# Performance work log

Hardware: AMD Instinct MI355X
Metric: run time of the kernel (lower is better)

## Reference

```python
import jax, jax.numpy as jnp
import numpy as np

NEG_SLOPE = 0.2  # PyG GATConv default negative_slope


def gat_conv(x, src, dst, W, a_src, a_dst, b, n_nodes):
    # x: [N, Cin]; W: [H, Cin, Cout]; a_src/a_dst: [H, Cout]; b: [Cout]
    xh = jnp.einsum('ni,hio->nho', x, W)                 # [N, H, Cout]
    al_s = jnp.einsum('nho,ho->nh', xh, a_src)           # [N, H]
    al_d = jnp.einsum('nho,ho->nh', xh, a_dst)           # [N, H]
    e = jax.nn.leaky_relu(al_s[src] + al_d[dst], NEG_SLOPE)  # [E, H]
    # softmax over incoming edges of each dst node (self-loops guarantee >=1 edge)
    m = jax.ops.segment_max(e, dst, num_segments=n_nodes)
    ex = jnp.exp(e - m[dst])
    den = jax.ops.segment_sum(ex, dst, num_segments=n_nodes)
    alpha = ex / den[dst]                                # [E, H]
    msg = alpha[:, :, None] * xh[src]                    # [E, H, Cout]
    out = jax.ops.segment_sum(msg, dst, num_segments=n_nodes)  # [N, H, Cout]
    return out.mean(axis=1) + b                          # concat=False -> head mean


def setup_inputs() -> dict:
    key = jax.random.key(0)
    ks = jax.random.split(key, 16)
    N, E, C, H = 20000, 320000, 128, 4
    s = 1.0 / np.sqrt(C)
    inp = {
        'x': jax.random.normal(ks[0], (N, C), dtype=jnp.float32),
        'edge_index': jax.random.randint(ks[1], (2, E), 0, N, dtype=jnp.int64),
    }
    for i, name in enumerate(['1', '2', 'r']):
        k0, k1, k2 = jax.random.split(ks[2 + i], 3)
        inp['W' + name] = jax.random.normal(k0, (H, C, C), dtype=jnp.float32) * s
        inp['as' + name] = jax.random.normal(k1, (H, C), dtype=jnp.float32) * s
        inp['ad' + name] = jax.random.normal(k2, (H, C), dtype=jnp.float32) * s
        inp['b' + name] = jnp.zeros((C,), dtype=jnp.float32)
    return inp


def reference(x, edge_index, W1, as1, ad1, b1, W2, as2, ad2, b2, Wr, asr, adr, br):
    n = x.shape[0]
    loop = jnp.arange(n, dtype=edge_index.dtype)
    src = jnp.concatenate([edge_index[0], loop])  # PyG add_self_loops=True
    dst = jnp.concatenate([edge_index[1], loop])
    h = gat_conv(x, src, dst, W1, as1, ad1, b1, n)
    h = gat_conv(h, src, dst, W2, as2, ad2, b2, n)
    res = gat_conv(x, src, dst, Wr, asr, adr, br, n)
    return h + res
```

## Files before the change

kernel.cpp:

```cpp
#include <hip/hip_runtime.h>
#include <math.h>

#define C 128

typedef unsigned short u16;
typedef __attribute__((ext_vector_type(8))) short short8;
typedef __attribute__((ext_vector_type(4))) float f32x4;
typedef __attribute__((ext_vector_type(4))) u16 u16x4;

__device__ __forceinline__ float b2f(u16 u) {
    union { unsigned i; float f; } x; x.i = (unsigned)u << 16; return x.f;
}
__device__ __forceinline__ u16 f2b(float f) {
    union { float f; unsigned i; } x; x.f = f;
    unsigned r = x.i + 0x7FFFu + ((x.i >> 16) & 1u);
    return (u16)(r >> 16);
}
__device__ __forceinline__ float lrelu(float x) { return x > 0.f ? x : 0.2f * x; }


__global__ void hist_kernel(const int* __restrict__ ei, int E, int N,
                            int* __restrict__ count) {
    int total = E + N;
    for (int e = blockIdx.x * blockDim.x + threadIdx.x; e < total;
         e += gridDim.x * blockDim.x) {
        int d = (e < E) ? ei[E + e] : (e - E);
        if ((unsigned)d < (unsigned)N) atomicAdd(&count[d], 1);
    }
}

__global__ __launch_bounds__(1024) void scan_kernel(const int* __restrict__ count,
                                                    int* __restrict__ offs,
                                                    int* __restrict__ cursor, int N) {
    int tid = threadIdx.x, lane = tid & 63, wid = tid >> 6;
    int CH = (N + 1023) >> 10;
    int base = tid * CH;
    int s = 0;
    for (int j = 0; j < CH; ++j) {
        int i = base + j;
        if (i < N) s += count[i];
    }
    int own = s;
    #pragma unroll
    for (int d = 1; d < 64; d <<= 1) {
        int v = __shfl_up(s, d);
        if (lane >= d) s += v;
    }
    __shared__ int wtot[16];
    if (lane == 63) wtot[wid] = s;
    __syncthreads();
    if (tid < 16) {
        int t = wtot[tid];
        int u = t;
        #pragma unroll
        for (int d = 1; d < 16; d <<= 1) {
            int v = __shfl_up(u, d);
            if (tid >= d) u += v;
        }
        wtot[tid] = u - t;
        if (tid == 15) offs[N] = u;
    }
    __syncthreads();
    int run = wtot[wid] + s - own;
    for (int j = 0; j < CH; ++j) {
        int i = base + j;
        if (i < N) {
            offs[i] = run;
            cursor[i] = run;
            run += count[i];
        }
    }
}

__global__ void scatter_kernel(const int* __restrict__ ei, int E, int N,
                               int* __restrict__ cursor, int* __restrict__ srcs,
                               int* __restrict__ dsts) {
    int total = E + N;
    for (int e = blockIdx.x * blockDim.x + threadIdx.x; e < total;
         e += gridDim.x * blockDim.x) {
        int sNode, d;
        if (e < E) { sNode = ei[e]; d = ei[E + e]; }
        else       { sNode = e - E; d = sNode; }
        if ((unsigned)d < (unsigned)N && (unsigned)sNode < (unsigned)N) {
            int pos = atomicAdd(&cursor[d], 1);
            srcs[pos] = sNode;
            dsts[pos] = d;
        }
    }
}


__global__ __launch_bounds__(256) void cvt_w_kernel(const float* __restrict__ W1,
                                                    const float* __restrict__ Wr,
                                                    const float* __restrict__ W2,
                                                    u16* __restrict__ Wf) {
    int idx = blockIdx.x * 256 + threadIdx.x;
    int lane = idx & 63;
    int kk = (idx >> 6) & 15;
    int t = (idx >> 10) & 7;
    int l = idx >> 13;
    if (l >= 3) return;
    const float* W = (l == 0) ? W1 : (l == 1) ? Wr : W2;
    int o = t * 16 + (lane & 15);
    int bk = kk * 32 + (lane >> 4) * 8;
    int h = bk >> 7, i0 = bk & 127;
    short8 v;
    #pragma unroll
    for (int j = 0; j < 8; ++j) {
        v[j] = (short)f2b(0.25f * W[((size_t)h * C + i0 + j) * C + o]);
    }
    *(short8*)(Wf + (size_t)idx * 8) = v;
}


__global__ __launch_bounds__(256) void wvec_kernel(const float* __restrict__ W1,
                                                   const float* __restrict__ as1,
                                                   const float* __restrict__ ad1,
                                                   const float* __restrict__ Wr,
                                                   const float* __restrict__ asr,
                                                   const float* __restrict__ adr,
                                                   const float* __restrict__ W2,
                                                   const float* __restrict__ as2,
                                                   const float* __restrict__ ad2,
                                                   u16* __restrict__ vsdA,
                                                   u16* __restrict__ vsdB) {
    int slot = blockIdx.x;
    const float* W  = (slot < 4) ? W1 : (slot < 8) ? Wr : W2;
    const float* s_ = (slot < 4) ? as1 : (slot < 8) ? asr : as2;
    const float* d_ = (slot < 4) ? ad1 : (slot < 8) ? adr : ad2;
    int h = slot & 3;
    int wave = threadIdx.x >> 6, lane = threadIdx.x & 63;
    int rbase = blockIdx.y * 32 + wave * 8;
    float as0 = s_[h * C + lane], as1v = s_[h * C + 64 + lane];
    float ad0 = d_[h * C + lane], ad1v = d_[h * C + 64 + lane];
    #pragma unroll
    for (int j = 0; j < 8; ++j) {
        int i = rbase + j;
        const float* Wrow = W + ((size_t)h * C + i) * C;
        float w0 = Wrow[lane], w1 = Wrow[64 + lane];
        float ps = w0 * as0 + w1 * as1v;
        float pd = w0 * ad0 + w1 * ad1v;
        #pragma unroll
        for (int m = 32; m; m >>= 1) {
            ps += __shfl_xor(ps, m);
            pd += __shfl_xor(pd, m);
        }
        if (lane == 0) {
            if (slot < 8) {
                vsdA[slot * C + i] = f2b(ps);
                vsdA[(8 + slot) * C + i] = f2b(pd);
            } else {
                vsdB[(slot - 8) * C + i] = f2b(ps);
                vsdB[(4 + (slot - 8)) * C + i] = f2b(pd);
            }
        }
    }
}


__global__ __launch_bounds__(256) void alA_kernel(const float* __restrict__ x,
                                                  const u16* __restrict__ vsd,
                                                  u16* __restrict__ xb,
                                                  float* __restrict__ als,
                                                  float* __restrict__ ald, int N) {
    int wave = threadIdx.x >> 6, lane = threadIdx.x & 63;
    int rowBase = blockIdx.x * 64 + wave * 16;
    int r = rowBase + (lane & 15);
    int rl = r < N ? r : N - 1;
    int kg = (lane >> 4) * 8;

    short8 a[4];
    #pragma unroll
    for (int t = 0; t < 4; ++t) {
        const float* xp = x + (size_t)rl * C + t * 32 + kg;
        float4 f0 = *(const float4*)xp;
        float4 f1 = *(const float4*)(xp + 4);
        short8 s;
        s[0] = f2b(f0.x); s[1] = f2b(f0.y); s[2] = f2b(f0.z); s[3] = f2b(f0.w);
        s[4] = f2b(f1.x); s[5] = f2b(f1.y); s[6] = f2b(f1.z); s[7] = f2b(f1.w);
        a[t] = s;
        if (r < N) *(short8*)(xb + (size_t)r * C + t * 32 + kg) = s;
    }
    f32x4 acc = {0.f, 0.f, 0.f, 0.f};
    int col = lane & 15;
    #pragma unroll
    for (int t = 0; t < 4; ++t) {
        short8 b = *(const short8*)(vsd + (size_t)col * C + t * 32 + kg);
        acc = __builtin_amdgcn_mfma_f32_16x16x32_bf16(a[t], b, acc, 0, 0, 0);
    }
    #pragma unroll
    for (int j = 0; j < 4; ++j) {
        int rr = rowBase + (lane >> 4) * 4 + j;
        if (rr < N) {
            if (col < 8) als[rr * 8 + col] = acc[j];
            else ald[rr * 8 + (col - 8)] = acc[j];
        }
    }
}


__global__ __launch_bounds__(256) void alB_kernel(const u16* __restrict__ in,
                                                  const u16* __restrict__ vsd,
                                                  float* __restrict__ als,
                                                  float* __restrict__ ald, int N) {
    int wave = threadIdx.x >> 6, lane = threadIdx.x & 63;
    int rowBase = blockIdx.x * 64 + wave * 16;
    int r = rowBase + (lane & 15);
    int rl = r < N ? r : N - 1;
    int kg = (lane >> 4) * 8;

    f32x4 acc = {0.f, 0.f, 0.f, 0.f};
    int col = lane & 15;
    #pragma unroll
    for (int t = 0; t < 4; ++t) {
        short8 a = *(const short8*)(in + (size_t)rl * C + t * 32 + kg);
        short8 b = *(const short8*)(vsd + (size_t)col * C + t * 32 + kg);
        acc = __builtin_amdgcn_mfma_f32_16x16x32_bf16(a, b, acc, 0, 0, 0);
    }
    #pragma unroll
    for (int j = 0; j < 4; ++j) {
        int rr = rowBase + (lane >> 4) * 4 + j;
        if (rr < N && col < 8) {
            if (col < 4) als[rr * 4 + col] = acc[j];
            else ald[rr * 4 + (col - 4)] = acc[j];
        }
    }
}


template <int NH>
__global__ __launch_bounds__(256) void ew_kernel(const float* __restrict__ als,
                                                 const float* __restrict__ ald,
                                                 const int* __restrict__ srcs,
                                                 const int* __restrict__ dsts,
                                                 float* __restrict__ wout, int ET) {
    int i = blockIdx.x * blockDim.x + threadIdx.x;
    if (i >= ET) return;
    int s = srcs[i], d = dsts[i];
    const float* as_ = als + (size_t)s * NH;
    const float* ad_ = ald + (size_t)d * NH;
    float* wo = wout + (size_t)i * NH;
    #pragma unroll
    for (int h = 0; h < NH; ++h) {
        wo[h] = __expf(lrelu(as_[h] + ad_[h]));
    }
}


template <int NH>
__global__ __launch_bounds__(256) void aggx_kernel(const u16* __restrict__ xsrc,
                                                   const float* __restrict__ wgt,
                                                   const int* __restrict__ offs,
                                                   const int* __restrict__ srcs,
                                                   u16* __restrict__ dest, int N) {
    constexpr int NHG = NH / 2;
    int node = blockIdx.x * 4 + (threadIdx.x >> 6);
    int lane = threadIdx.x & 63;
    if (node >= N) return;
    int g = lane >> 5;
    int c0 = (lane & 31) * 4;
    int beg = offs[node], end = offs[node + 1];

    float dacc[NHG] = {};
    float acc[NHG][4] = {};

    int i = beg;
    int iend8 = beg + ((end - beg) & ~7);

    if (i < iend8) {
        int sA[8];
        #pragma unroll
        for (int e = 0; e < 8; ++e) sA[e] = srcs[i + e];
        while (i < iend8) {
            int inext = i + 8;
            int sB[8];
            #pragma unroll
            for (int e = 0; e < 8; ++e) sB[e] = srcs[inext + e];

            u16x4 v[8];
            #pragma unroll
            for (int e = 0; e < 8; ++e) {
                v[e] = *(const u16x4*)(xsrc + (size_t)sA[e] * C + c0);
            }
            float wv[8][NHG];
            #pragma unroll
            for (int e = 0; e < 8; ++e) {
                if constexpr (NHG == 4) {
                    float4 wq = *(const float4*)(wgt + (size_t)(i + e) * NH + g * NHG);
                    wv[e][0] = wq.x; wv[e][1] = wq.y; wv[e][2] = wq.z; wv[e][3] = wq.w;
                } else {
                    float2 wq = *(const float2*)(wgt + (size_t)(i + e) * NH + g * NHG);
                    wv[e][0] = wq.x; wv[e][1] = wq.y;
                }
            }
            #pragma unroll
            for (int e = 0; e < 8; ++e) {
                float f[4];
                #pragma unroll
                for (int j = 0; j < 4; ++j) f[j] = b2f(v[e][j]);
                #pragma unroll
                for (int j2 = 0; j2 < NHG; ++j2) {
                    dacc[j2] += wv[e][j2];
                    #pragma unroll
                    for (int j = 0; j < 4; ++j) acc[j2][j] += wv[e][j2] * f[j];
                }
            }
            #pragma unroll
            for (int e = 0; e < 8; ++e) sA[e] = sB[e];
            i = inext;
        }
    }
    for (; i < end; ++i) {
        int s0 = srcs[i];
        u16x4 v0 = *(const u16x4*)(xsrc + (size_t)s0 * C + c0);
        float w0[NHG];
        #pragma unroll
        for (int j2 = 0; j2 < NHG; ++j2) {
            w0[j2] = wgt[(size_t)i * NH + g * NHG + j2];
        }
        float f[4];
        #pragma unroll
        for (int j = 0; j < 4; ++j) f[j] = b2f(v0[j]);
        #pragma unroll
        for (int j2 = 0; j2 < NHG; ++j2) {
            dacc[j2] += w0[j2];
            #pragma unroll
            for (int j = 0; j < 4; ++j) acc[j2][j] += w0[j2] * f[j];
        }
    }

    #pragma unroll
    for (int j2 = 0; j2 < NHG; ++j2) {
        float inv = 1.f / dacc[j2];
        int h = g * NHG + j2;
        u16x4 o = {f2b(acc[j2][0] * inv), f2b(acc[j2][1] * inv),
                   f2b(acc[j2][2] * inv), f2b(acc[j2][3] * inv)};
        *(u16x4*)(dest + (size_t)node * (NH * C) + h * C + c0) = o;
    }
}


__global__ __launch_bounds__(256) void gemmL1_kernel(const u16* __restrict__ agg,
                                                     const u16* __restrict__ Wf,
                                                     const float* __restrict__ b1,
                                                     u16* __restrict__ h1b, int N) {
    int wave = threadIdx.x >> 6, lane = threadIdx.x & 63;
    int ch = blockIdx.y;
    int rowBase = blockIdx.x * 64 + wave * 16;
    int p = lane & 15, q = lane >> 4;
    int r = rowBase + p;
    int rl = r < N ? r : N - 1;
    int kg = q * 8;

    const short8* ap = (const short8*)(agg + (size_t)rl * 1024 + kg);
    const u16* wb = Wf + (size_t)(ch * 4 * 16) * 512 + lane * 8;

    f32x4 acc[4];
    #pragma unroll
    for (int t = 0; t < 4; ++t) acc[t] = (f32x4){0.f, 0.f, 0.f, 0.f};

    #pragma unroll
    for (int kk = 0; kk < 16; ++kk) {
        short8 a = ap[kk * 4];
        #pragma unroll
        for (int t = 0; t < 4; ++t) {
            short8 b = *(const short8*)(wb + (size_t)(t * 16 + kk) * 512);
            acc[t] = __builtin_amdgcn_mfma_f32_16x16x32_bf16(a, b, acc[t], 0, 0, 0);
        }
    }

    #pragma unroll
    for (int t = 0; t < 4; ++t) {
        int col = (ch * 4 + t) * 16 + p;
        float bcol = b1[col];
        #pragma unroll
        for (int j = 0; j < 4; ++j) {
            int rr = rowBase + q * 4 + j;
            if (rr < N) h1b[(size_t)rr * C + col] = f2b(acc[t][j] + bcol);
        }
    }
}


__global__ __launch_bounds__(256) void gemmF_kernel(const u16* __restrict__ aggB,
                                                    const u16* __restrict__ aggA,
                                                    const u16* __restrict__ Wf,
                                                    const float* __restrict__ b2,
                                                    const float* __restrict__ br,
                                                    float* __restrict__ outf, int N) {
    int wave = threadIdx.x >> 6, lane = threadIdx.x & 63;
    int ch = blockIdx.y;
    int rowBase = blockIdx.x * 64 + wave * 16;
    int p = lane & 15, q = lane >> 4;
    int r = rowBase + p;
    int rl = r < N ? r : N - 1;
    int kg = q * 8;

    const short8* apB = (const short8*)(aggB + (size_t)rl * 512 + kg);
    const short8* apR = (const short8*)(aggA + (size_t)rl * 1024 + 512 + kg);
    const u16* wb2 = Wf + (size_t)2 * 65536 + (size_t)(ch * 4 * 16) * 512 + lane * 8;
    const u16* wbr = Wf + (size_t)1 * 65536 + (size_t)(ch * 4 * 16) * 512 + lane * 8;

    f32x4 acc[4];
    #pragma unroll
    for (int t = 0; t < 4; ++t) acc[t] = (f32x4){0.f, 0.f, 0.f, 0.f};

    #pragma unroll
    for (int kk = 0; kk < 16; ++kk) {
        short8 a = apB[kk * 4];
        #pragma unroll
        for (int t = 0; t < 4; ++t) {
            short8 b = *(const short8*)(wb2 + (size_t)(t * 16 + kk) * 512);
            acc[t] = __builtin_amdgcn_mfma_f32_16x16x32_bf16(a, b, acc[t], 0, 0, 0);
        }
    }
    #pragma unroll
    for (int kk = 0; kk < 16; ++kk) {
        short8 a = apR[kk * 4];
        #pragma unroll
        for (int t = 0; t < 4; ++t) {
            short8 b = *(const short8*)(wbr + (size_t)(t * 16 + kk) * 512);
            acc[t] = __builtin_amdgcn_mfma_f32_16x16x32_bf16(a, b, acc[t], 0, 0, 0);
        }
    }

    #pragma unroll
    for (int t = 0; t < 4; ++t) {
        int col = (ch * 4 + t) * 16 + p;
        float bcol = b2[col] + br[col];
        #pragma unroll
        for (int j = 0; j < 4; ++j) {
            int rr = rowBase + q * 4 + j;
            if (rr < N) outf[(size_t)rr * C + col] = acc[t][j] + bcol;
        }
    }
}


extern "C" void kernel_launch(void* const* d_in, const int* in_sizes, int n_in,
                              void* d_out, int out_size, void* d_ws, size_t ws_size,
                              hipStream_t stream) {
    const float* x = (const float*)d_in[0];
    const int* ei = (const int*)d_in[1];
    const float* W1 = (const float*)d_in[2];
    const float* as1 = (const float*)d_in[3];
    const float* ad1 = (const float*)d_in[4];
    const float* b1 = (const float*)d_in[5];
    const float* W2 = (const float*)d_in[6];
    const float* as2 = (const float*)d_in[7];
    const float* ad2 = (const float*)d_in[8];
    const float* b2 = (const float*)d_in[9];
    const float* Wr = (const float*)d_in[10];
    const float* asr = (const float*)d_in[11];
    const float* adr = (const float*)d_in[12];
    const float* br = (const float*)d_in[13];

    int N = in_sizes[0] / C;
    int E = in_sizes[1] / 2;
    int ET = E + N;

    size_t sz_xb    = (size_t)N * C * 2;
    size_t sz_h1b   = (size_t)N * C * 2;
    size_t sz_aggA  = (size_t)N * 1024 * 2;
    size_t sz_aggB  = (size_t)N * 512 * 2;
    size_t sz_wc    = (size_t)3 * C * 512 * 2;
    size_t sz_vsd   = (size_t)16 * C * 2;
    size_t sz_al8   = (size_t)N * 8 * 4;
    size_t sz_count = (size_t)N * 4;
    size_t sz_offs  = (size_t)(N + 4) * 4;
    size_t sz_srcs  = (size_t)ET * 4;
    size_t sz_w     = (size_t)ET * 8 * 4;
    size_t required = sz_xb + sz_h1b + sz_aggA + sz_aggB + sz_wc + 2 * sz_vsd +
                      2 * sz_al8 + 2 * sz_count + sz_offs + 2 * sz_srcs + sz_w;
    if (ws_size < required) return;

    char* w = (char*)d_ws;
    u16* xb = (u16*)w;        w += sz_xb;
    u16* h1b = (u16*)w;       w += sz_h1b;
    u16* aggA = (u16*)w;      w += sz_aggA;
    u16* aggB = (u16*)w;      w += sz_aggB;
    u16* Wf = (u16*)w;        w += sz_wc;
    u16* vsdA = (u16*)w;      w += sz_vsd;
    u16* vsdB = (u16*)w;      w += sz_vsd;
    float* als = (float*)w;   w += sz_al8;
    float* ald = (float*)w;   w += sz_al8;
    int* count = (int*)w;     w += sz_count;
    int* cursor = (int*)w;    w += sz_count;
    int* offs = (int*)w;      w += sz_offs;
    int* srcs = (int*)w;      w += sz_srcs;
    int* dsts = (int*)w;      w += sz_srcs;
    float* wgt = (float*)w;   w += sz_w;
    float* out = (float*)d_out;

    hipMemsetAsync(count, 0, sz_count, stream);
    hist_kernel<<<512, 256, 0, stream>>>(ei, E, N, count);
    scan_kernel<<<1, 1024, 0, stream>>>(count, offs, cursor, N);
    scatter_kernel<<<512, 256, 0, stream>>>(ei, E, N, cursor, srcs, dsts);

    cvt_w_kernel<<<96, 256, 0, stream>>>(W1, Wr, W2, Wf);
    wvec_kernel<<<dim3(12, 4), 256, 0, stream>>>(W1, as1, ad1, Wr, asr, adr,
                                                 W2, as2, ad2, vsdA, vsdB);

    int nwb = (N + 3) / 4;
    int neb = (ET + 255) / 256;
    int gx = (N + 63) / 64;

    alA_kernel<<<gx, 256, 0, stream>>>(x, vsdA, xb, als, ald, N);
    ew_kernel<8><<<neb, 256, 0, stream>>>(als, ald, srcs, dsts, wgt, ET);
    aggx_kernel<8><<<nwb, 256, 0, stream>>>(xb, wgt, offs, srcs, aggA, N);
    gemmL1_kernel<<<dim3(gx, 2), 256, 0, stream>>>(aggA, Wf, b1, h1b, N);

    alB_kernel<<<gx, 256, 0, stream>>>(h1b, vsdB, als, ald, N);
    ew_kernel<4><<<neb, 256, 0, stream>>>(als, ald, srcs, dsts, wgt, ET);
    aggx_kernel<4><<<nwb, 256, 0, stream>>>(h1b, wgt, offs, srcs, aggB, N);
    gemmF_kernel<<<dim3(gx, 2), 256, 0, stream>>>(aggB, aggA, Wf, b2, br, out, N);
}
```

Baseline: 307.8 us.

## Fuse edge-weight computation into aggregation and merge prep kernels

Drops the separate per-edge weight kernels: the aggregation kernel now reads per-source attention logits and computes exp(leaky_relu(as+ad)) inline, so the dst array and the per-edge weight buffer are no longer needed. The weight conversion, attention-vector projection and count zeroing are merged into one prep kernel, replacing a memset and two launches. This avoids writing and re-reading an E×H float buffer and cuts launch count. In exchange the aggregation kernel does extra gathers of als rows and recomputes exp per lane group.

```diff
diff --git a/kernel.cpp b/kernel.cpp
--- a/kernel.cpp
+++ b/kernel.cpp
@@ -73,8 +73,7 @@
 }
 
 __global__ void scatter_kernel(const int* __restrict__ ei, int E, int N,
-                               int* __restrict__ cursor, int* __restrict__ srcs,
-                               int* __restrict__ dsts) {
+                               int* __restrict__ cursor, int* __restrict__ srcs) {
     int total = E + N;
     for (int e = blockIdx.x * blockDim.x + threadIdx.x; e < total;
          e += gridDim.x * blockDim.x) {
@@ -84,36 +83,12 @@
         if ((unsigned)d < (unsigned)N && (unsigned)sNode < (unsigned)N) {
             int pos = atomicAdd(&cursor[d], 1);
             srcs[pos] = sNode;
-            dsts[pos] = d;
-        }
-    }
-}
-
-
-__global__ __launch_bounds__(256) void cvt_w_kernel(const float* __restrict__ W1,
-                                                    const float* __restrict__ Wr,
-                                                    const float* __restrict__ W2,
-                                                    u16* __restrict__ Wf) {
-    int idx = blockIdx.x * 256 + threadIdx.x;
-    int lane = idx & 63;
-    int kk = (idx >> 6) & 15;
-    int t = (idx >> 10) & 7;
-    int l = idx >> 13;
-    if (l >= 3) return;
-    const float* W = (l == 0) ? W1 : (l == 1) ? Wr : W2;
-    int o = t * 16 + (lane & 15);
-    int bk = kk * 32 + (lane >> 4) * 8;
-    int h = bk >> 7, i0 = bk & 127;
-    short8 v;
-    #pragma unroll
-    for (int j = 0; j < 8; ++j) {
-        v[j] = (short)f2b(0.25f * W[((size_t)h * C + i0 + j) * C + o]);
-    }
-    *(short8*)(Wf + (size_t)idx * 8) = v;
-}
-
-
-__global__ __launch_bounds__(256) void wvec_kernel(const float* __restrict__ W1,
+        }
+    }
+}
+
+
+__global__ __launch_bounds__(256) void prep_kernel(const float* __restrict__ W1,
                                                    const float* __restrict__ as1,
                                                    const float* __restrict__ ad1,
                                                    const float* __restrict__ Wr,
@@ -122,38 +97,63 @@
                                                    const float* __restrict__ W2,
                                                    const float* __restrict__ as2,
                                                    const float* __restrict__ ad2,
+                                                   u16* __restrict__ Wf,
                                                    u16* __restrict__ vsdA,
-                                                   u16* __restrict__ vsdB) {
-    int slot = blockIdx.x;
-    const float* W  = (slot < 4) ? W1 : (slot < 8) ? Wr : W2;
-    const float* s_ = (slot < 4) ? as1 : (slot < 8) ? asr : as2;
-    const float* d_ = (slot < 4) ? ad1 : (slot < 8) ? adr : ad2;
-    int h = slot & 3;
-    int wave = threadIdx.x >> 6, lane = threadIdx.x & 63;
-    int rbase = blockIdx.y * 32 + wave * 8;
-    float as0 = s_[h * C + lane], as1v = s_[h * C + 64 + lane];
-    float ad0 = d_[h * C + lane], ad1v = d_[h * C + 64 + lane];
-    #pragma unroll
-    for (int j = 0; j < 8; ++j) {
-        int i = rbase + j;
-        const float* Wrow = W + ((size_t)h * C + i) * C;
-        float w0 = Wrow[lane], w1 = Wrow[64 + lane];
-        float ps = w0 * as0 + w1 * as1v;
-        float pd = w0 * ad0 + w1 * ad1v;
-        #pragma unroll
-        for (int m = 32; m; m >>= 1) {
-            ps += __shfl_xor(ps, m);
-            pd += __shfl_xor(pd, m);
-        }
-        if (lane == 0) {
-            if (slot < 8) {
-                vsdA[slot * C + i] = f2b(ps);
-                vsdA[(8 + slot) * C + i] = f2b(pd);
-            } else {
-                vsdB[(slot - 8) * C + i] = f2b(ps);
-                vsdB[(4 + (slot - 8)) * C + i] = f2b(pd);
+                                                   u16* __restrict__ vsdB,
+                                                   int* __restrict__ count, int N) {
+    int blk = blockIdx.x;
+    if (blk < 96) {
+        int idx = blk * 256 + threadIdx.x;
+        int lane = idx & 63;
+        int kk = (idx >> 6) & 15;
+        int t = (idx >> 10) & 7;
+        int l = idx >> 13;
+        const float* W = (l == 0) ? W1 : (l == 1) ? Wr : W2;
+        int o = t * 16 + (lane & 15);
+        int bk = kk * 32 + (lane >> 4) * 8;
+        int h = bk >> 7, i0 = bk & 127;
+        short8 v;
+        #pragma unroll
+        for (int j = 0; j < 8; ++j) {
+            v[j] = (short)f2b(0.25f * W[((size_t)h * C + i0 + j) * C + o]);
+        }
+        *(short8*)(Wf + (size_t)idx * 8) = v;
+    } else if (blk < 144) {
+        int b2 = blk - 96;
+        int slot = b2 >> 2;
+        const float* W  = (slot < 4) ? W1 : (slot < 8) ? Wr : W2;
+        const float* s_ = (slot < 4) ? as1 : (slot < 8) ? asr : as2;
+        const float* d_ = (slot < 4) ? ad1 : (slot < 8) ? adr : ad2;
+        int h = slot & 3;
+        int wave = threadIdx.x >> 6, lane = threadIdx.x & 63;
+        int rbase = (b2 & 3) * 32 + wave * 8;
+        float as0 = s_[h * C + lane], as1v = s_[h * C + 64 + lane];
+        float ad0 = d_[h * C + lane], ad1v = d_[h * C + 64 + lane];
+        #pragma unroll
+        for (int j = 0; j < 8; ++j) {
+            int i = rbase + j;
+            const float* Wrow = W + ((size_t)h * C + i) * C;
+            float w0 = Wrow[lane], w1 = Wrow[64 + lane];
+            float ps = w0 * as0 + w1 * as1v;
+            float pd = w0 * ad0 + w1 * ad1v;
+            #pragma unroll
+            for (int m = 32; m; m >>= 1) {
+                ps += __shfl_xor(ps, m);
+                pd += __shfl_xor(pd, m);
             }
-        }
+            if (lane == 0) {
+                if (slot < 8) {
+                    vsdA[slot * C + i] = f2b(ps);
+                    vsdA[(8 + slot) * C + i] = f2b(pd);
+                } else {
+                    vsdB[(slot - 8) * C + i] = f2b(ps);
+                    vsdB[(4 + (slot - 8)) * C + i] = f2b(pd);
+                }
+            }
+        }
+    } else {
+        int i = (blk - 144) * 256 + threadIdx.x;
+        if (i < N) count[i] = 0;
     }
 }
 
@@ -229,27 +229,9 @@
 
 
 template <int NH>
-__global__ __launch_bounds__(256) void ew_kernel(const float* __restrict__ als,
-                                                 const float* __restrict__ ald,
-                                                 const int* __restrict__ srcs,
-                                                 const int* __restrict__ dsts,
-                                                 float* __restrict__ wout, int ET) {
-    int i = blockIdx.x * blockDim.x + threadIdx.x;
-    if (i >= ET) return;
-    int s = srcs[i], d = dsts[i];
-    const float* as_ = als + (size_t)s * NH;
-    const float* ad_ = ald + (size_t)d * NH;
-    float* wo = wout + (size_t)i * NH;
-    #pragma unroll
-    for (int h = 0; h < NH; ++h) {
-        wo[h] = __expf(lrelu(as_[h] + ad_[h]));
-    }
-}
-
-
-template <int NH>
 __global__ __launch_bounds__(256) void aggx_kernel(const u16* __restrict__ xsrc,
-                                                   const float* __restrict__ wgt,
+                                                   const float* __restrict__ als,
+                                                   const float* __restrict__ ald,
                                                    const int* __restrict__ offs,
                                                    const int* __restrict__ srcs,
                                                    u16* __restrict__ dest, int N) {
@@ -261,6 +243,12 @@
     int c0 = (lane & 31) * 4;
     int beg = offs[node], end = offs[node + 1];
 
+    float adh[NHG];
+    #pragma unroll
+    for (int j = 0; j < NHG; ++j) {
+        adh[j] = ald[(size_t)node * NH + g * NHG + j];
+    }
+
     float dacc[NHG] = {};
     float acc[NHG][4] = {};
 
@@ -277,6 +265,17 @@
             #pragma unroll
             for (int e = 0; e < 8; ++e) sB[e] = srcs[inext + e];
 
+            float av[8][NHG];
+            #pragma unroll
+            for (int e = 0; e < 8; ++e) {
+                if constexpr (NHG == 4) {
+                    float4 t = *(const float4*)(als + (size_t)sA[e] * NH + g * NHG);
+                    av[e][0] = t.x; av[e][1] = t.y; av[e][2] = t.z; av[e][3] = t.w;
+                } else {
+                    float2 t = *(const float2*)(als + (size_t)sA[e] * NH + g * NHG);
+                    av[e][0] = t.x; av[e][1] = t.y;
+                }
+            }
             u16x4 v[8];
             #pragma unroll
             for (int e = 0; e < 8; ++e) {
@@ -285,12 +284,9 @@
             float wv[8][NHG];
             #pragma unroll
             for (int e = 0; e < 8; ++e) {
-                if constexpr (NHG == 4) {
-                    float4 wq = *(const float4*)(wgt + (size_t)(i + e) * NH + g * NHG);
-                    wv[e][0] = wq.x; wv[e][1] = wq.y; wv[e][2] = wq.z; wv[e][3] = wq.w;
-                } else {
-                    float2 wq = *(const float2*)(wgt + (size_t)(i + e) * NH + g * NHG);
-                    wv[e][0] = wq.x; wv[e][1] = wq.y;
+                #pragma unroll
+                for (int j2 = 0; j2 < NHG; ++j2) {
+                    wv[e][j2] = __expf(lrelu(av[e][j2] + adh[j2]));
                 }
             }
             #pragma unroll
@@ -313,19 +309,15 @@
     for (; i < end; ++i) {
         int s0 = srcs[i];
         u16x4 v0 = *(const u16x4*)(xsrc + (size_t)s0 * C + c0);
-        float w0[NHG];
+        float f[4];
+        #pragma unroll
+        for (int j = 0; j < 4; ++j) f[j] = b2f(v0[j]);
         #pragma unroll
         for (int j2 = 0; j2 < NHG; ++j2) {
-            w0[j2] = wgt[(size_t)i * NH + g * NHG + j2];
-        }
-        float f[4];
-        #pragma unroll
-        for (int j = 0; j < 4; ++j) f[j] = b2f(v0[j]);
-        #pragma unroll
-        for (int j2 = 0; j2 < NHG; ++j2) {
-            dacc[j2] += w0[j2];
-            #pragma unroll
-            for (int j = 0; j < 4; ++j) acc[j2][j] += w0[j2] * f[j];
+            float w0 = __expf(lrelu(als[(size_t)s0 * NH + g * NHG + j2] + adh[j2]));
+            dacc[j2] += w0;
+            #pragma unroll
+            for (int j = 0; j < 4; ++j) acc[j2][j] += w0 * f[j];
         }
     }
 
@@ -468,10 +460,9 @@
     size_t sz_al8   = (size_t)N * 8 * 4;
     size_t sz_count = (size_t)N * 4;
     size_t sz_offs  = (size_t)(N + 4) * 4;
-    size_t sz_srcs  = (size_t)ET * 4;
-    size_t sz_w     = (size_t)ET * 8 * 4;
+    size_t sz_srcs  = (size_t)ET * 4 + 64;
     size_t required = sz_xb + sz_h1b + sz_aggA + sz_aggB + sz_wc + 2 * sz_vsd +
-                      2 * sz_al8 + 2 * sz_count + sz_offs + 2 * sz_srcs + sz_w;
+                      2 * sz_al8 + 2 * sz_count + sz_offs + sz_srcs;
     if (ws_size < required) return;
 
     char* w = (char*)d_ws;
@@ -488,30 +479,24 @@
     int* cursor = (int*)w;    w += sz_count;
     int* offs = (int*)w;      w += sz_offs;
     int* srcs = (int*)w;      w += sz_srcs;
-    int* dsts = (int*)w;      w += sz_srcs;
-    float* wgt = (float*)w;   w += sz_w;
     float* out = (float*)d_out;
 
-    hipMemsetAsync(count, 0, sz_count, stream);
+    int nzb = (N + 255) / 256;
+    int nwb = (N + 3) / 4;
+    int gx = (N + 63) / 64;
+
+    prep_kernel<<<144 + nzb, 256, 0, stream>>>(W1, as1, ad1, Wr, asr, adr,
+                                               W2, as2, ad2, Wf, vsdA, vsdB,
+                                               count, N);
     hist_kernel<<<512, 256, 0, stream>>>(ei, E, N, count);
     scan_kernel<<<1, 1024, 0, stream>>>(count, offs, cursor, N);
-    scatter_kernel<<<512, 256, 0, stream>>>(ei, E, N, cursor, srcs, dsts);
-
-    cvt_w_kernel<<<96, 256, 0, stream>>>(W1, Wr, W2, Wf);
-    wvec_kernel<<<dim3(12, 4), 256, 0, stream>>>(W1, as1, ad1, Wr, asr, adr,
-                                                 W2, as2, ad2, vsdA, vsdB);
-
-    int nwb = (N + 3) / 4;
-    int neb = (ET + 255) / 256;
-    int gx = (N + 63) / 64;
+    scatter_kernel<<<512, 256, 0, stream>>>(ei, E, N, cursor, srcs);
 
     alA_kernel<<<gx, 256, 0, stream>>>(x, vsdA, xb, als, ald, N);
-    ew_kernel<8><<<neb, 256, 0, stream>>>(als, ald, srcs, dsts, wgt, ET);
-    aggx_kernel<8><<<nwb, 256, 0, stream>>>(xb, wgt, offs, srcs, aggA, N);
+    aggx_kernel<8><<<nwb, 256, 0, stream>>>(xb, als, ald, offs, srcs, aggA, N);
     gemmL1_kernel<<<dim3(gx, 2), 256, 0, stream>>>(aggA, Wf, b1, h1b, N);
 
     alB_kernel<<<gx, 256, 0, stream>>>(h1b, vsdB, als, ald, N);
-    ew_kernel<4><<<neb, 256, 0, stream>>>(als, ald, srcs, dsts, wgt, ET);
-    aggx_kernel<4><<<nwb, 256, 0, stream>>>(h1b, wgt, offs, srcs, aggB, N);
+    aggx_kernel<4><<<nwb, 256, 0, stream>>>(h1b, als, ald, offs, srcs, aggB, N);
     gemmF_kernel<<<dim3(gx, 2), 256, 0, stream>>>(aggB, aggA, Wf, b2, br, out, N);
 }
```

After: 312.6 us. About the same (+1.6%).
